# Performance work log

Measured on AMD Instinct MI355X. Metric: run time of the kernel, lower is better.

Reference implementation:

```python
import jax, jax.numpy as jnp
import numpy as np

B = 256        # trees per batch
DEPTH = 10     # complete binary tree depth -> 2^10 - 1 = 1023 internal nodes
N = 2**DEPTH - 1
IN = 128       # input_size
H = 128        # hidden_size
C = 5          # num_classes


def setup_inputs() -> dict:
    key = jax.random.key(0)
    ks = jax.random.split(key, 13)
    gdim = IN + 2 * H  # concat(x, h_left, h_right)
    inp = {"x": jax.random.normal(ks[0], (B, N, IN), jnp.float32)}
    names = ["i", "fl", "fr", "o", "u"]
    for j, nm in enumerate(names):
        inp[f"W_{nm}"] = 0.05 * jax.random.normal(ks[1 + 2 * j], (H, gdim), jnp.float32)
        inp[f"b_{nm}"] = 0.05 * jax.random.normal(ks[2 + 2 * j], (H,), jnp.float32)
    inp["W_cls"] = 0.05 * jax.random.normal(ks[11], (C, H), jnp.float32)
    inp["b_cls"] = 0.05 * jax.random.normal(ks[12], (C,), jnp.float32)
    return inp


def reference(x, W_i, b_i, W_fl, b_fl, W_fr, b_fr, W_o, b_o, W_u, b_u, W_cls, b_cls):
    # Level-order complete binary tree: node k has children 2k+1, 2k+2.
    # Bottom-up sweep; below the deepest internal level all children are
    # empty nodes with h = c = 0 (matches the original base case).
    Bb = x.shape[0]
    h = jnp.zeros((Bb, 2 ** DEPTH, H), x.dtype)
    c = jnp.zeros_like(h)
    for d in range(DEPTH - 1, -1, -1):  # fixed, small structural loop
        n = 2 ** d
        start = n - 1  # level-order offset of level d
        xs = x[:, start:start + n]            # [B, n, IN]
        hl, hr = h[:, 0::2], h[:, 1::2]       # children of node j are 2j, 2j+1 (level-local)
        cl, cr = c[:, 0::2], c[:, 1::2]
        comb = jnp.concatenate([xs, hl, hr], axis=-1)  # [B, n, IN+2H]
        lin = lambda W, b: jnp.einsum('bng,og->bno', comb, W) + b
        i = jax.nn.sigmoid(lin(W_i, b_i))
        fl = jax.nn.sigmoid(lin(W_fl, b_fl))
        fr = jax.nn.sigmoid(lin(W_fr, b_fr))
        o = jax.nn.sigmoid(lin(W_o, b_o))
        u = jnp.tanh(lin(W_u, b_u))
        c = i * u + fl * cl + fr * cr
        h = o * jnp.tanh(c)
    root_h = h[:, 0]                          # [B, H]
    logits = root_h @ W_cls.T + b_cls         # [B, C]
    return logits
```

## Files before the change

kernel.cpp:

```cpp
#include <hip/hip_runtime.h>
#include <hip/hip_bf16.h>
#include <stdint.h>


#define BATCH 256
#define NTOT 1023
#define HDIM 128
#define NCLS 5
#define GDIM 384

typedef __bf16 bf16x8 __attribute__((ext_vector_type(8)));
typedef float f32x4 __attribute__((ext_vector_type(4)));

__device__ __forceinline__ float sigmoid_f(float v) { return 1.f / (1.f + __expf(-v)); }
__device__ __forceinline__ float tanh_f(float v) { return 1.f - 2.f / (1.f + __expf(2.f * v)); }

__device__ __forceinline__ void load_lds16(const void* g, void* l) {
  __builtin_amdgcn_global_load_lds((const __attribute__((address_space(1))) unsigned int*)g,
                                   (__attribute__((address_space(3))) unsigned int*)l, 16, 0, 0);
}

__global__ __launch_bounds__(256) void pack_w(
    const float* __restrict__ W0, const float* __restrict__ W1, const float* __restrict__ W2,
    const float* __restrict__ W3, const float* __restrict__ W4, __bf16* __restrict__ PW)
{
  int t = blockIdx.x * 256 + threadIdx.x;
  int lane = t & 63;
  int chunk = t >> 6;
  int ks = chunk % 12;
  int jf = (chunk / 12) & 7;
  int g = chunk / 96;
  const float* W = (g == 0) ? W0 : (g == 1) ? W1 : (g == 2) ? W2 : (g == 3) ? W3 : W4;
  const float* s = W + (size_t)(jf * 16 + (lane & 15)) * GDIM + ks * 32 + (lane >> 4) * 8;
  float4 v0 = *(const float4*)s;
  float4 v1 = *(const float4*)(s + 4);
  bf16x8 w;
  w[0] = (__bf16)v0.x; w[1] = (__bf16)v0.y; w[2] = (__bf16)v0.z; w[3] = (__bf16)v0.w;
  w[4] = (__bf16)v1.x; w[5] = (__bf16)v1.y; w[6] = (__bf16)v1.z; w[7] = (__bf16)v1.w;
  *(bf16x8*)(PW + (size_t)t * 8) = w;
}

#define TB_P  81920
#define TB_Q  132096
#define CSTR  132

template<int NMF, bool LEAF, bool LAST>
__device__ __forceinline__ void fused_level(
    const float* __restrict__ xp,
    const __bf16* __restrict__ PW,
    const float* __restrict__ bv0, const float* __restrict__ bv1,
    const float* __restrict__ bv2, const float* __restrict__ bv3,
    const float* __restrict__ bv4,
    unsigned char* lds,
    const unsigned char* prev_h, const float* prev_c,
    unsigned char* cur_h, float* cur_c,
    __bf16* __restrict__ gh, float* __restrict__ gc,
    int nvalid)
{
  const int tid = threadIdx.x;
  const int w = tid >> 6;
  const int l = tid & 63;
  const int l15 = l & 15;
  const int quad = l >> 4;
  const int q8 = quad * 8;
  constexpr int NACC = LEAF ? 3 : 5;
  constexpr int NKT = LEAF ? 4 : 12;
  constexpr int NCH = NACC * 8;
  constexpr int NQ = NCH / 8;

  auto stageB = [&](int ks) {
    unsigned char* Bb = lds + (ks & 1) * 40960;
#pragma unroll
    for (int q = 0; q < NQ; ++q) {
      int c = w * NQ + q;
      int ai = c >> 3, jf = c & 7;
      int g = LEAF ? (ai ? ai + 2 : 0) : ai;
      const __bf16* src = PW + (((size_t)(g * 8 + jf) * 12 + ks) * 64 + l) * 8;
      load_lds16(src, Bb + c * 1024);
    }
  };

  stageB(0);

  bf16x8 xf[NMF][4];
#pragma unroll
  for (int mf = 0; mf < NMF; ++mf) {
    const float* xr = xp + (size_t)(mf * 16 + l15) * HDIM + q8;
#pragma unroll
    for (int kx = 0; kx < 4; ++kx) {
      float4 v0 = *(const float4*)(xr + kx * 32);
      float4 v1 = *(const float4*)(xr + kx * 32 + 4);
      bf16x8 t;
      t[0] = (__bf16)v0.x; t[1] = (__bf16)v0.y; t[2] = (__bf16)v0.z; t[3] = (__bf16)v0.w;
      t[4] = (__bf16)v1.x; t[5] = (__bf16)v1.y; t[6] = (__bf16)v1.z; t[7] = (__bf16)v1.w;
      xf[mf][kx] = t;
    }
  }

  f32x4 acc[NMF][NACC];
#pragma unroll
  for (int mf = 0; mf < NMF; ++mf)
#pragma unroll
    for (int ai = 0; ai < NACC; ++ai)
      acc[mf][ai] = (f32x4){0.f, 0.f, 0.f, 0.f};

#pragma unroll
  for (int ks = 0; ks < NKT; ++ks) {
    __syncthreads();
    if (ks + 1 < NKT) stageB(ks + 1);
    const unsigned char* Bb = lds + (ks & 1) * 40960;
    bf16x8 a[NMF];
#pragma unroll
    for (int mf = 0; mf < NMF; ++mf) {
      if (LEAF || ks < 4) {
        a[mf] = xf[mf][LEAF ? ks : (ks & 3)];
      } else {
        const int o = (ks < 8) ? 0 : 1;
        const int col2 = ((ks - (o ? 8 : 4)) * 32 + q8) * 2;
        const int n = 2 * (mf * 16 + l15) + o;
        a[mf] = *(const bf16x8*)(prev_h + n * 256 + (col2 ^ ((n & 7) << 4)));
      }
    }
#pragma unroll
    for (int ai = 0; ai < NACC; ++ai) {
      bf16x8 bb = *(const bf16x8*)(Bb + (ai * 8 + w) * 1024 + l * 16);
#pragma unroll
      for (int mf = 0; mf < NMF; ++mf)
        acc[mf][ai] = __builtin_amdgcn_mfma_f32_16x16x32_bf16(a[mf], bb, acc[mf][ai], 0, 0, 0);
    }
  }

  const int je = w * 16 + l15;
  const float b0 = bv0[je], b3v = bv3[je], b4v = bv4[je];
#pragma unroll
  for (int mf = 0; mf < NMF; ++mf) {
#pragma unroll
    for (int r = 0; r < 4; ++r) {
      const int me = mf * 16 + quad * 4 + r;
      if (me < nvalid) {
        float gi = sigmoid_f(acc[mf][0][r] + b0);
        float go = sigmoid_f(acc[mf][LEAF ? 1 : 3][r] + b3v);
        float gu = tanh_f(acc[mf][LEAF ? 2 : 4][r] + b4v);
        float cv = gi * gu;
        if constexpr (!LEAF) {
          float gl = sigmoid_f(acc[mf][1][r] + bv1[je]);
          float gr = sigmoid_f(acc[mf][2][r] + bv2[je]);
          cv += gl * prev_c[(2 * me) * CSTR + je] + gr * prev_c[(2 * me + 1) * CSTR + je];
        }
        float hv = go * tanh_f(cv);
        if constexpr (LAST) {
          gc[(size_t)me * HDIM + je] = cv;
          gh[(size_t)me * HDIM + je] = (__bf16)hv;
        } else {
          cur_c[me * CSTR + je] = cv;
          *(__bf16*)(cur_h + me * 256 + ((je * 2) ^ ((me & 7) << 4))) = (__bf16)hv;
        }
      }
    }
  }
}

__global__ __launch_bounds__(512, 1) void fused_top(
    const float* __restrict__ x, const __bf16* __restrict__ PW,
    const float* __restrict__ bv0, const float* __restrict__ bv1,
    const float* __restrict__ bv2, const float* __restrict__ bv3,
    const float* __restrict__ bv4,
    __bf16* __restrict__ h6, float* __restrict__ c6)
{
  __shared__ unsigned char lds[157184];
  const int b = blockIdx.x >> 3;
  const int s = blockIdx.x & 7;
  unsigned char* Ph = lds + TB_P;
  float* Pc = (float*)(lds + TB_P + 16384);
  unsigned char* Qh = lds + TB_Q;
  float* Qc = (float*)(lds + TB_Q + 8192);
  const size_t xb = (size_t)b * NTOT;

  fused_level<4, true, false>(x + (xb + 511 + s * 64) * HDIM, PW,
      bv0, bv1, bv2, bv3, bv4, lds, nullptr, nullptr, Ph, Pc, nullptr, nullptr, 64);
  fused_level<2, false, false>(x + (xb + 255 + s * 32) * HDIM, PW,
      bv0, bv1, bv2, bv3, bv4, lds, Ph, Pc, Qh, Qc, nullptr, nullptr, 32);
  fused_level<1, false, false>(x + (xb + 127 + s * 16) * HDIM, PW,
      bv0, bv1, bv2, bv3, bv4, lds, Qh, Qc, Ph, Pc, nullptr, nullptr, 16);
  fused_level<1, false, true>(x + (xb + 63 + s * 8) * HDIM, PW,
      bv0, bv1, bv2, bv3, bv4, lds, Ph, Pc, nullptr, nullptr,
      h6 + ((size_t)b * 64 + s * 8) * HDIM, c6 + ((size_t)b * 64 + s * 8) * HDIM, 8);
}

__global__ __launch_bounds__(256, 1) void tail_kernel(
    const float* __restrict__ x, const __bf16* __restrict__ PW,
    const float* __restrict__ bv0, const float* __restrict__ bv1,
    const float* __restrict__ bv2, const float* __restrict__ bv3,
    const float* __restrict__ bv4,
    const float* __restrict__ Wcls, const float* __restrict__ bcls,
    const __bf16* __restrict__ h6, const float* __restrict__ c6,
    float* __restrict__ out)
{
  __shared__ unsigned char lds[157184];
  const int b = blockIdx.x;
  const int tid = threadIdx.x;
  const int w = tid >> 6;
  const int l = tid & 63;
  const int l15 = l & 15;
  const int quad = l >> 4;
  const int q8 = quad * 8;

  unsigned char* Ph = lds + TB_P;
  float* Pc = (float*)(lds + TB_P + 16384);
  unsigned char* Qh = lds + TB_Q;
  float* Qc = (float*)(lds + TB_Q + 8192);

  {
    const __bf16* hs = h6 + (size_t)b * 64 * HDIM;
#pragma unroll
    for (int it = 0; it < 4; ++it) {
      int idx = it * 256 + tid;
      int node = idx >> 4, i8 = idx & 15;
      bf16x8 v = *(const bf16x8*)(hs + node * HDIM + i8 * 8);
      *(bf16x8*)(Ph + node * 256 + ((i8 * 16) ^ ((node & 7) << 4))) = v;
    }
    const float* cs = c6 + (size_t)b * 64 * HDIM;
#pragma unroll
    for (int it = 0; it < 8; ++it) {
      int idx = it * 256 + tid;
      int node = idx >> 5, seg = idx & 31;
      float4 v = *(const float4*)(cs + node * HDIM + seg * 4);
      *(float4*)(Pc + node * CSTR + seg * 4) = v;
    }
  }

  for (int d = 5; d >= 0; --d) {
    const int s = 5 - d;
    const int n = 1 << d;
    const int nmf = (d == 5) ? 2 : 1;
    unsigned char* prev_h = (s & 1) ? Qh : Ph;
    float*         prev_c = (s & 1) ? Qc : Pc;
    unsigned char* cur_h  = (s & 1) ? Ph : Qh;
    float*         cur_c  = (s & 1) ? Pc : Qc;

    bf16x8 xf[2][4];
#pragma unroll
    for (int mf = 0; mf < 2; ++mf) {
      const float* xr = x + ((size_t)b * NTOT + (n - 1) + mf * 16 + l15) * HDIM + q8;
#pragma unroll
      for (int ks = 0; ks < 4; ++ks) {
        float4 v0 = *(const float4*)(xr + ks * 32);
        float4 v1 = *(const float4*)(xr + ks * 32 + 4);
        bf16x8 t;
        t[0] = (__bf16)v0.x; t[1] = (__bf16)v0.y; t[2] = (__bf16)v0.z; t[3] = (__bf16)v0.w;
        t[4] = (__bf16)v1.x; t[5] = (__bf16)v1.y; t[6] = (__bf16)v1.z; t[7] = (__bf16)v1.w;
        xf[mf][ks] = t;
      }
    }

    auto stageB = [&](int ks) {
      unsigned char* Bb = lds + (ks & 1) * 40960;
#pragma unroll
      for (int q = 0; q < 10; ++q) {
        int c = w * 10 + q;
        const __bf16* src = PW + ((size_t)(c * 12 + ks) * 64 + l) * 8;
        load_lds16(src, Bb + c * 1024);
      }
    };

    f32x4 acc[2][2][5];
#pragma unroll
    for (int mf = 0; mf < 2; ++mf)
#pragma unroll
      for (int jfl = 0; jfl < 2; ++jfl)
#pragma unroll
        for (int g = 0; g < 5; ++g)
          acc[mf][jfl][g] = (f32x4){0.f, 0.f, 0.f, 0.f};

    stageB(0);
    for (int ks = 0; ks < 12; ++ks) {
      __syncthreads();
      if (ks < 11) stageB(ks + 1);
      const unsigned char* Bb = lds + (ks & 1) * 40960;
      bf16x8 a0, a1;
      if (ks < 4) {
        a0 = xf[0][ks];
        a1 = xf[1][ks];
      } else {
        const int o = (ks < 8) ? 0 : 1;
        const int col2 = (((ks - (o ? 8 : 4)) * 32) + q8) * 2;
        int n0 = 2 * l15 + o;
        int n1 = 2 * (16 + l15) + o;
        a0 = *(const bf16x8*)(prev_h + n0 * 256 + (col2 ^ ((n0 & 7) << 4)));
        a1 = *(const bf16x8*)(prev_h + n1 * 256 + (col2 ^ ((n1 & 7) << 4)));
      }
#pragma unroll
      for (int g = 0; g < 5; ++g) {
#pragma unroll
        for (int jfl = 0; jfl < 2; ++jfl) {
          bf16x8 bb = *(const bf16x8*)(Bb + (g * 8 + w * 2 + jfl) * 1024 + l * 16);
          acc[0][jfl][g] = __builtin_amdgcn_mfma_f32_16x16x32_bf16(a0, bb, acc[0][jfl][g], 0, 0, 0);
          if (nmf == 2)
            acc[1][jfl][g] = __builtin_amdgcn_mfma_f32_16x16x32_bf16(a1, bb, acc[1][jfl][g], 0, 0, 0);
        }
      }
    }

#pragma unroll
    for (int jfl = 0; jfl < 2; ++jfl) {
      const int je = w * 32 + jfl * 16 + l15;
      const float b0 = bv0[je], b1 = bv1[je], b2 = bv2[je], b3 = bv3[je], b4 = bv4[je];
#pragma unroll
      for (int mf = 0; mf < 2; ++mf) {
#pragma unroll
        for (int r = 0; r < 4; ++r) {
          const int me = mf * 16 + quad * 4 + r;
          if (me < n) {
            float gi = sigmoid_f(acc[mf][jfl][0][r] + b0);
            float gl = sigmoid_f(acc[mf][jfl][1][r] + b1);
            float gr = sigmoid_f(acc[mf][jfl][2][r] + b2);
            float go = sigmoid_f(acc[mf][jfl][3][r] + b3);
            float gu = tanh_f(acc[mf][jfl][4][r] + b4);
            float cv = gi * gu + gl * prev_c[(2 * me) * CSTR + je]
                               + gr * prev_c[(2 * me + 1) * CSTR + je];
            cur_c[me * CSTR + je] = cv;
            *(__bf16*)(cur_h + me * 256 + ((je * 2) ^ ((me & 7) << 4))) =
                (__bf16)(go * tanh_f(cv));
          }
        }
      }
    }
  }

  __syncthreads();
  if (tid < NCLS) {
    float sacc = bcls[tid];
    for (int k = 0; k < HDIM; ++k)
      sacc += (float)(*(const __bf16*)(Ph + k * 2)) * Wcls[tid * HDIM + k];
    out[(size_t)b * NCLS + tid] = sacc;
  }
}

extern "C" void kernel_launch(void* const* d_in, const int* in_sizes, int n_in,
                              void* d_out, int out_size, void* d_ws, size_t ws_size,
                              hipStream_t stream) {
  const float* x  = (const float*)d_in[0];
  const float* W[5]  = {(const float*)d_in[1], (const float*)d_in[3], (const float*)d_in[5],
                        (const float*)d_in[7], (const float*)d_in[9]};
  const float* bv[5] = {(const float*)d_in[2], (const float*)d_in[4], (const float*)d_in[6],
                        (const float*)d_in[8], (const float*)d_in[10]};
  const float* Wcls = (const float*)d_in[11];
  const float* bcls = (const float*)d_in[12];

  uint8_t* ws = (uint8_t*)d_ws;
  __bf16* hb1 = (__bf16*)(ws + 33554432);
  float*  cb1 = (float*)(ws + 117440512);
  __bf16* PW  = (__bf16*)(ws + 150994944);

  pack_w<<<120, 256, 0, stream>>>(W[0], W[1], W[2], W[3], W[4], PW);

  fused_top<<<BATCH * 8, 512, 0, stream>>>(
      x, PW, bv[0], bv[1], bv[2], bv[3], bv[4], hb1, cb1);

  tail_kernel<<<BATCH, 256, 0, stream>>>(
      x, PW, bv[0], bv[1], bv[2], bv[3], bv[4],
      Wcls, bcls, hb1, cb1, (float*)d_out);
}
```

Baseline: 565.7 us.

## Give each wave private double-buffered weight staging with vmcnt waits instead of block barriers

Each wave now stages into its own LDS region only the weight chunks it consumes, so the per-k-step __syncthreads is removed. Progress is tracked with explicit s_waitcnt vmcnt/lgkmcnt and the pipeline prefetches two k-steps ahead. Explicit barriers are added between levels so the h/c exchange stays correct. The intent is to remove block-wide synchronisation stalls in the MFMA loop and deepen load overlap, at the cost of relying on hand-counted wait numbers that must match the issued loads.

```diff
diff --git a/kernel.cpp b/kernel.cpp
--- a/kernel.cpp
+++ b/kernel.cpp
@@ -18,6 +18,16 @@
 __device__ __forceinline__ void load_lds16(const void* g, void* l) {
   __builtin_amdgcn_global_load_lds((const __attribute__((address_space(1))) unsigned int*)g,
                                    (__attribute__((address_space(3))) unsigned int*)l, 16, 0, 0);
+}
+
+template<int N>
+__device__ __forceinline__ void wait_vm() {
+  asm volatile("s_waitcnt vmcnt(%0)" :: "i"(N) : "memory");
+  __builtin_amdgcn_sched_barrier(0);
+}
+__device__ __forceinline__ void wait_lgkm0() {
+  asm volatile("s_waitcnt lgkmcnt(0)" ::: "memory");
+  __builtin_amdgcn_sched_barrier(0);
 }
 
 __global__ __launch_bounds__(256) void pack_w(
@@ -65,22 +75,20 @@
   const int q8 = quad * 8;
   constexpr int NACC = LEAF ? 3 : 5;
   constexpr int NKT = LEAF ? 4 : 12;
-  constexpr int NCH = NACC * 8;
-  constexpr int NQ = NCH / 8;
-
-  auto stageB = [&](int ks) {
-    unsigned char* Bb = lds + (ks & 1) * 40960;
-#pragma unroll
-    for (int q = 0; q < NQ; ++q) {
-      int c = w * NQ + q;
-      int ai = c >> 3, jf = c & 7;
-      int g = LEAF ? (ai ? ai + 2 : 0) : ai;
-      const __bf16* src = PW + (((size_t)(g * 8 + jf) * 12 + ks) * 64 + l) * 8;
-      load_lds16(src, Bb + c * 1024);
+  unsigned char* Bw = lds + w * 10240;
+
+  auto stage = [&](int ks) {
+    unsigned char* Bb = Bw + (ks & 1) * 5120;
+#pragma unroll
+    for (int q = 0; q < NACC; ++q) {
+      int g = LEAF ? (q ? q + 2 : 0) : q;
+      const __bf16* src = PW + (((size_t)(g * 8 + w) * 12 + ks) * 64 + l) * 8;
+      load_lds16(src, Bb + q * 1024);
     }
   };
 
-  stageB(0);
+  stage(0);
+  stage(1);
 
   bf16x8 xf[NMF][4];
 #pragma unroll
@@ -106,9 +114,12 @@
 
 #pragma unroll
   for (int ks = 0; ks < NKT; ++ks) {
-    __syncthreads();
-    if (ks + 1 < NKT) stageB(ks + 1);
-    const unsigned char* Bb = lds + (ks & 1) * 40960;
+    if (ks < NKT - 1) wait_vm<NACC>(); else wait_vm<0>();
+    const unsigned char* Bb = Bw + (ks & 1) * 5120;
+    bf16x8 bb[NACC];
+#pragma unroll
+    for (int q = 0; q < NACC; ++q)
+      bb[q] = *(const bf16x8*)(Bb + q * 1024 + l * 16);
     bf16x8 a[NMF];
 #pragma unroll
     for (int mf = 0; mf < NMF; ++mf) {
@@ -117,16 +128,18 @@
       } else {
         const int o = (ks < 8) ? 0 : 1;
         const int col2 = ((ks - (o ? 8 : 4)) * 32 + q8) * 2;
-        const int n = 2 * (mf * 16 + l15) + o;
-        a[mf] = *(const bf16x8*)(prev_h + n * 256 + (col2 ^ ((n & 7) << 4)));
-      }
-    }
-#pragma unroll
-    for (int ai = 0; ai < NACC; ++ai) {
-      bf16x8 bb = *(const bf16x8*)(Bb + (ai * 8 + w) * 1024 + l * 16);
+        const int nn = 2 * (mf * 16 + l15) + o;
+        a[mf] = *(const bf16x8*)(prev_h + nn * 256 + (col2 ^ ((nn & 7) << 4)));
+      }
+    }
+#pragma unroll
+    for (int q = 0; q < NACC; ++q)
 #pragma unroll
       for (int mf = 0; mf < NMF; ++mf)
-        acc[mf][ai] = __builtin_amdgcn_mfma_f32_16x16x32_bf16(a[mf], bb, acc[mf][ai], 0, 0, 0);
+        acc[mf][q] = __builtin_amdgcn_mfma_f32_16x16x32_bf16(a[mf], bb[q], acc[mf][q], 0, 0, 0);
+    if (ks + 2 < NKT) {
+      wait_lgkm0();
+      stage(ks + 2);
     }
   }
 
@@ -178,10 +191,13 @@
 
   fused_level<4, true, false>(x + (xb + 511 + s * 64) * HDIM, PW,
       bv0, bv1, bv2, bv3, bv4, lds, nullptr, nullptr, Ph, Pc, nullptr, nullptr, 64);
+  __syncthreads();
   fused_level<2, false, false>(x + (xb + 255 + s * 32) * HDIM, PW,
       bv0, bv1, bv2, bv3, bv4, lds, Ph, Pc, Qh, Qc, nullptr, nullptr, 32);
+  __syncthreads();
   fused_level<1, false, false>(x + (xb + 127 + s * 16) * HDIM, PW,
       bv0, bv1, bv2, bv3, bv4, lds, Qh, Qc, Ph, Pc, nullptr, nullptr, 16);
+  __syncthreads();
   fused_level<1, false, true>(x + (xb + 63 + s * 8) * HDIM, PW,
       bv0, bv1, bv2, bv3, bv4, lds, Ph, Pc, nullptr, nullptr,
       h6 + ((size_t)b * 64 + s * 8) * HDIM, c6 + ((size_t)b * 64 + s * 8) * HDIM, 8);
@@ -228,6 +244,7 @@
       *(float4*)(Pc + node * CSTR + seg * 4) = v;
     }
   }
+  __syncthreads();
 
   for (int d = 5; d >= 0; --d) {
     const int s = 5 - d;
@@ -237,6 +254,20 @@
     float*         prev_c = (s & 1) ? Qc : Pc;
     unsigned char* cur_h  = (s & 1) ? Ph : Qh;
     float*         cur_c  = (s & 1) ? Pc : Qc;
+    unsigned char* Bw = lds + w * 20480;
+
+    auto stageB = [&](int ks) {
+      unsigned char* Bb = Bw + (ks & 1) * 10240;
+#pragma unroll
+      for (int q = 0; q < 10; ++q) {
+        int g = q >> 1, jfl = q & 1;
+        const __bf16* src = PW + (((size_t)(g * 8 + w * 2 + jfl) * 12 + ks) * 64 + l) * 8;
+        load_lds16(src, Bb + q * 1024);
+      }
+    };
+
+    stageB(0);
+    stageB(1);
 
     bf16x8 xf[2][4];
 #pragma unroll
@@ -253,16 +284,6 @@
       }
     }
 
-    auto stageB = [&](int ks) {
-      unsigned char* Bb = lds + (ks & 1) * 40960;
-#pragma unroll
-      for (int q = 0; q < 10; ++q) {
-        int c = w * 10 + q;
-        const __bf16* src = PW + ((size_t)(c * 12 + ks) * 64 + l) * 8;
-        load_lds16(src, Bb + c * 1024);
-      }
-    };
-
     f32x4 acc[2][2][5];
 #pragma unroll
     for (int mf = 0; mf < 2; ++mf)
@@ -272,11 +293,10 @@
         for (int g = 0; g < 5; ++g)
           acc[mf][jfl][g] = (f32x4){0.f, 0.f, 0.f, 0.f};
 
-    stageB(0);
+#pragma unroll
     for (int ks = 0; ks < 12; ++ks) {
-      __syncthreads();
-      if (ks < 11) stageB(ks + 1);
-      const unsigned char* Bb = lds + (ks & 1) * 40960;
+      if (ks < 11) wait_vm<10>(); else wait_vm<0>();
+      const unsigned char* Bb = Bw + (ks & 1) * 10240;
       bf16x8 a0, a1;
       if (ks < 4) {
         a0 = xf[0][ks];
@@ -293,11 +313,15 @@
       for (int g = 0; g < 5; ++g) {
 #pragma unroll
         for (int jfl = 0; jfl < 2; ++jfl) {
-          bf16x8 bb = *(const bf16x8*)(Bb + (g * 8 + w * 2 + jfl) * 1024 + l * 16);
-          acc[0][jfl][g] = __builtin_amdgcn_mfma_f32_16x16x32_bf16(a0, bb, acc[0][jfl][g], 0, 0, 0);
+          bf16x8 bbv = *(const bf16x8*)(Bb + (g * 2 + jfl) * 1024 + l * 16);
+          acc[0][jfl][g] = __builtin_amdgcn_mfma_f32_16x16x32_bf16(a0, bbv, acc[0][jfl][g], 0, 0, 0);
           if (nmf == 2)
-            acc[1][jfl][g] = __builtin_amdgcn_mfma_f32_16x16x32_bf16(a1, bb, acc[1][jfl][g], 0, 0, 0);
+            acc[1][jfl][g] = __builtin_amdgcn_mfma_f32_16x16x32_bf16(a1, bbv, acc[1][jfl][g], 0, 0, 0);
         }
+      }
+      if (ks + 2 < 12) {
+        wait_lgkm0();
+        stageB(ks + 2);
       }
     }
 
@@ -325,9 +349,9 @@
         }
       }
     }
-  }
-
-  __syncthreads();
+    __syncthreads();
+  }
+
   if (tid < NCLS) {
     float sacc = bcls[tid];
     for (int k = 0; k < HDIM; ++k)
```

New measurement: 554.9 us. About the same (-1.9%).

## Load weight fragments directly into registers and shrink LDS to raise occupancy

Applied to the files above, without the earlier changes.

Weight B-fragments are no longer staged through double-buffered LDS via global_load_lds. Each wave now loads its fragments straight from global memory into registers, with a two-deep prefetch, and x fragments are streamed the same way. This cuts LDS use to about 75KB, so launch bounds can allow several blocks per CU, and the per-k-step __syncthreads is removed. The tail kernel is rewritten to 512 threads and reuses the shared fused_level routine. The risks are more register pressure and redundant weight loads from L2 across waves and blocks.

```diff
diff --git a/kernel.cpp b/kernel.cpp
--- a/kernel.cpp
+++ b/kernel.cpp
@@ -14,11 +14,6 @@
 
 __device__ __forceinline__ float sigmoid_f(float v) { return 1.f / (1.f + __expf(-v)); }
 __device__ __forceinline__ float tanh_f(float v) { return 1.f - 2.f / (1.f + __expf(2.f * v)); }
-
-__device__ __forceinline__ void load_lds16(const void* g, void* l) {
-  __builtin_amdgcn_global_load_lds((const __attribute__((address_space(1))) unsigned int*)g,
-                                   (__attribute__((address_space(3))) unsigned int*)l, 16, 0, 0);
-}
 
 __global__ __launch_bounds__(256) void pack_w(
     const float* __restrict__ W0, const float* __restrict__ W1, const float* __restrict__ W2,
@@ -40,9 +35,9 @@
   *(bf16x8*)(PW + (size_t)t * 8) = w;
 }
 
-#define TB_P  81920
-#define TB_Q  132096
-#define CSTR  132
+#define LDS_TOT 75264
+#define Q_OFF   50176
+#define CSTR    132
 
 template<int NMF, bool LEAF, bool LAST>
 __device__ __forceinline__ void fused_level(
@@ -51,7 +46,6 @@
     const float* __restrict__ bv0, const float* __restrict__ bv1,
     const float* __restrict__ bv2, const float* __restrict__ bv3,
     const float* __restrict__ bv4,
-    unsigned char* lds,
     const unsigned char* prev_h, const float* prev_c,
     unsigned char* cur_h, float* cur_c,
     __bf16* __restrict__ gh, float* __restrict__ gc,
@@ -65,69 +59,66 @@
   const int q8 = quad * 8;
   constexpr int NACC = LEAF ? 3 : 5;
   constexpr int NKT = LEAF ? 4 : 12;
-  constexpr int NCH = NACC * 8;
-  constexpr int NQ = NCH / 8;
-
-  auto stageB = [&](int ks) {
-    unsigned char* Bb = lds + (ks & 1) * 40960;
-#pragma unroll
-    for (int q = 0; q < NQ; ++q) {
-      int c = w * NQ + q;
-      int ai = c >> 3, jf = c & 7;
-      int g = LEAF ? (ai ? ai + 2 : 0) : ai;
-      const __bf16* src = PW + (((size_t)(g * 8 + jf) * 12 + ks) * 64 + l) * 8;
-      load_lds16(src, Bb + c * 1024);
+
+  const bf16x8* PB = (const bf16x8*)PW;
+
+  bf16x8 bb[2][NACC];
+  bf16x8 xb[2][NMF];
+
+  auto loadB = [&](int buf, int ks) {
+#pragma unroll
+    for (int q = 0; q < NACC; ++q) {
+      const int g = LEAF ? (q ? q + 2 : 0) : q;
+      bb[buf][q] = PB[((size_t)(g * 8 + w) * 12 + ks) * 64 + l];
     }
   };
-
-  stageB(0);
-
-  bf16x8 xf[NMF][4];
-#pragma unroll
-  for (int mf = 0; mf < NMF; ++mf) {
-    const float* xr = xp + (size_t)(mf * 16 + l15) * HDIM + q8;
-#pragma unroll
-    for (int kx = 0; kx < 4; ++kx) {
-      float4 v0 = *(const float4*)(xr + kx * 32);
-      float4 v1 = *(const float4*)(xr + kx * 32 + 4);
+  auto loadX = [&](int buf, int kx) {
+#pragma unroll
+    for (int mf = 0; mf < NMF; ++mf) {
+      const float* xr = xp + (size_t)(mf * 16 + l15) * HDIM + q8 + kx * 32;
+      float4 v0 = *(const float4*)xr;
+      float4 v1 = *(const float4*)(xr + 4);
       bf16x8 t;
       t[0] = (__bf16)v0.x; t[1] = (__bf16)v0.y; t[2] = (__bf16)v0.z; t[3] = (__bf16)v0.w;
       t[4] = (__bf16)v1.x; t[5] = (__bf16)v1.y; t[6] = (__bf16)v1.z; t[7] = (__bf16)v1.w;
-      xf[mf][kx] = t;
-    }
-  }
+      xb[buf][mf] = t;
+    }
+  };
+
+  loadB(0, 0);
+  loadX(0, 0);
+  loadB(1, 1);
+  loadX(1, 1);
 
   f32x4 acc[NMF][NACC];
 #pragma unroll
   for (int mf = 0; mf < NMF; ++mf)
 #pragma unroll
-    for (int ai = 0; ai < NACC; ++ai)
-      acc[mf][ai] = (f32x4){0.f, 0.f, 0.f, 0.f};
+    for (int q = 0; q < NACC; ++q)
+      acc[mf][q] = (f32x4){0.f, 0.f, 0.f, 0.f};
 
 #pragma unroll
   for (int ks = 0; ks < NKT; ++ks) {
-    __syncthreads();
-    if (ks + 1 < NKT) stageB(ks + 1);
-    const unsigned char* Bb = lds + (ks & 1) * 40960;
+    const int cb = ks & 1;
     bf16x8 a[NMF];
 #pragma unroll
     for (int mf = 0; mf < NMF; ++mf) {
       if (LEAF || ks < 4) {
-        a[mf] = xf[mf][LEAF ? ks : (ks & 3)];
+        a[mf] = xb[cb][mf];
       } else {
         const int o = (ks < 8) ? 0 : 1;
         const int col2 = ((ks - (o ? 8 : 4)) * 32 + q8) * 2;
-        const int n = 2 * (mf * 16 + l15) + o;
-        a[mf] = *(const bf16x8*)(prev_h + n * 256 + (col2 ^ ((n & 7) << 4)));
+        const int nn = 2 * (mf * 16 + l15) + o;
+        a[mf] = *(const bf16x8*)(prev_h + nn * 256 + (col2 ^ ((nn & 7) << 4)));
       }
     }
 #pragma unroll
-    for (int ai = 0; ai < NACC; ++ai) {
-      bf16x8 bb = *(const bf16x8*)(Bb + (ai * 8 + w) * 1024 + l * 16);
+    for (int q = 0; q < NACC; ++q)
 #pragma unroll
       for (int mf = 0; mf < NMF; ++mf)
-        acc[mf][ai] = __builtin_amdgcn_mfma_f32_16x16x32_bf16(a[mf], bb, acc[mf][ai], 0, 0, 0);
-    }
+        acc[mf][q] = __builtin_amdgcn_mfma_f32_16x16x32_bf16(a[mf], bb[cb][q], acc[mf][q], 0, 0, 0);
+    if (ks + 2 < NKT) loadB(cb, ks + 2);
+    if (ks + 2 < 4)   loadX(cb, ks + 2);
   }
 
   const int je = w * 16 + l15;
@@ -160,34 +151,37 @@
   }
 }
 
-__global__ __launch_bounds__(512, 1) void fused_top(
+__global__ __launch_bounds__(512, 4) void fused_top(
     const float* __restrict__ x, const __bf16* __restrict__ PW,
     const float* __restrict__ bv0, const float* __restrict__ bv1,
     const float* __restrict__ bv2, const float* __restrict__ bv3,
     const float* __restrict__ bv4,
     __bf16* __restrict__ h6, float* __restrict__ c6)
 {
-  __shared__ unsigned char lds[157184];
+  __shared__ unsigned char lds[LDS_TOT];
   const int b = blockIdx.x >> 3;
   const int s = blockIdx.x & 7;
-  unsigned char* Ph = lds + TB_P;
-  float* Pc = (float*)(lds + TB_P + 16384);
-  unsigned char* Qh = lds + TB_Q;
-  float* Qc = (float*)(lds + TB_Q + 8192);
+  unsigned char* Ph = lds;
+  float* Pc = (float*)(lds + 16384);
+  unsigned char* Qh = lds + Q_OFF;
+  float* Qc = (float*)(lds + Q_OFF + 8192);
   const size_t xb = (size_t)b * NTOT;
 
   fused_level<4, true, false>(x + (xb + 511 + s * 64) * HDIM, PW,
-      bv0, bv1, bv2, bv3, bv4, lds, nullptr, nullptr, Ph, Pc, nullptr, nullptr, 64);
+      bv0, bv1, bv2, bv3, bv4, nullptr, nullptr, Ph, Pc, nullptr, nullptr, 64);
+  __syncthreads();
   fused_level<2, false, false>(x + (xb + 255 + s * 32) * HDIM, PW,
-      bv0, bv1, bv2, bv3, bv4, lds, Ph, Pc, Qh, Qc, nullptr, nullptr, 32);
+      bv0, bv1, bv2, bv3, bv4, Ph, Pc, Qh, Qc, nullptr, nullptr, 32);
+  __syncthreads();
   fused_level<1, false, false>(x + (xb + 127 + s * 16) * HDIM, PW,
-      bv0, bv1, bv2, bv3, bv4, lds, Qh, Qc, Ph, Pc, nullptr, nullptr, 16);
+      bv0, bv1, bv2, bv3, bv4, Qh, Qc, Ph, Pc, nullptr, nullptr, 16);
+  __syncthreads();
   fused_level<1, false, true>(x + (xb + 63 + s * 8) * HDIM, PW,
-      bv0, bv1, bv2, bv3, bv4, lds, Ph, Pc, nullptr, nullptr,
+      bv0, bv1, bv2, bv3, bv4, Ph, Pc, nullptr, nullptr,
       h6 + ((size_t)b * 64 + s * 8) * HDIM, c6 + ((size_t)b * 64 + s * 8) * HDIM, 8);
 }
 
-__global__ __launch_bounds__(256, 1) void tail_kernel(
+__global__ __launch_bounds__(512, 4) void tail_kernel(
     const float* __restrict__ x, const __bf16* __restrict__ PW,
     const float* __restrict__ bv0, const float* __restrict__ bv1,
     const float* __restrict__ bv2, const float* __restrict__ bv3,
@@ -196,138 +190,54 @@
     const __bf16* __restrict__ h6, const float* __restrict__ c6,
     float* __restrict__ out)
 {
-  __shared__ unsigned char lds[157184];
+  __shared__ unsigned char lds[LDS_TOT];
   const int b = blockIdx.x;
   const int tid = threadIdx.x;
-  const int w = tid >> 6;
-  const int l = tid & 63;
-  const int l15 = l & 15;
-  const int quad = l >> 4;
-  const int q8 = quad * 8;
-
-  unsigned char* Ph = lds + TB_P;
-  float* Pc = (float*)(lds + TB_P + 16384);
-  unsigned char* Qh = lds + TB_Q;
-  float* Qc = (float*)(lds + TB_Q + 8192);
+  unsigned char* Ph = lds;
+  float* Pc = (float*)(lds + 16384);
+  unsigned char* Qh = lds + Q_OFF;
+  float* Qc = (float*)(lds + Q_OFF + 8192);
 
   {
     const __bf16* hs = h6 + (size_t)b * 64 * HDIM;
 #pragma unroll
-    for (int it = 0; it < 4; ++it) {
-      int idx = it * 256 + tid;
+    for (int it = 0; it < 2; ++it) {
+      int idx = it * 512 + tid;
       int node = idx >> 4, i8 = idx & 15;
       bf16x8 v = *(const bf16x8*)(hs + node * HDIM + i8 * 8);
       *(bf16x8*)(Ph + node * 256 + ((i8 * 16) ^ ((node & 7) << 4))) = v;
     }
     const float* cs = c6 + (size_t)b * 64 * HDIM;
 #pragma unroll
-    for (int it = 0; it < 8; ++it) {
-      int idx = it * 256 + tid;
+    for (int it = 0; it < 4; ++it) {
+      int idx = it * 512 + tid;
       int node = idx >> 5, seg = idx & 31;
       float4 v = *(const float4*)(cs + node * HDIM + seg * 4);
       *(float4*)(Pc + node * CSTR + seg * 4) = v;
     }
   }
-
-  for (int d = 5; d >= 0; --d) {
-    const int s = 5 - d;
-    const int n = 1 << d;
-    const int nmf = (d == 5) ? 2 : 1;
-    unsigned char* prev_h = (s & 1) ? Qh : Ph;
-    float*         prev_c = (s & 1) ? Qc : Pc;
-    unsigned char* cur_h  = (s & 1) ? Ph : Qh;
-    float*         cur_c  = (s & 1) ? Pc : Qc;
-
-    bf16x8 xf[2][4];
-#pragma unroll
-    for (int mf = 0; mf < 2; ++mf) {
-      const float* xr = x + ((size_t)b * NTOT + (n - 1) + mf * 16 + l15) * HDIM + q8;
-#pragma unroll
-      for (int ks = 0; ks < 4; ++ks) {
-        float4 v0 = *(const float4*)(xr + ks * 32);
-        float4 v1 = *(const float4*)(xr + ks * 32 + 4);
-        bf16x8 t;
-        t[0] = (__bf16)v0.x; t[1] = (__bf16)v0.y; t[2] = (__bf16)v0.z; t[3] = (__bf16)v0.w;
-        t[4] = (__bf16)v1.x; t[5] = (__bf16)v1.y; t[6] = (__bf16)v1.z; t[7] = (__bf16)v1.w;
-        xf[mf][ks] = t;
-      }
-    }
-
-    auto stageB = [&](int ks) {
-      unsigned char* Bb = lds + (ks & 1) * 40960;
-#pragma unroll
-      for (int q = 0; q < 10; ++q) {
-        int c = w * 10 + q;
-        const __bf16* src = PW + ((size_t)(c * 12 + ks) * 64 + l) * 8;
-        load_lds16(src, Bb + c * 1024);
-      }
-    };
-
-    f32x4 acc[2][2][5];
-#pragma unroll
-    for (int mf = 0; mf < 2; ++mf)
-#pragma unroll
-      for (int jfl = 0; jfl < 2; ++jfl)
-#pragma unroll
-        for (int g = 0; g < 5; ++g)
-          acc[mf][jfl][g] = (f32x4){0.f, 0.f, 0.f, 0.f};
-
-    stageB(0);
-    for (int ks = 0; ks < 12; ++ks) {
-      __syncthreads();
-      if (ks < 11) stageB(ks + 1);
-      const unsigned char* Bb = lds + (ks & 1) * 40960;
-      bf16x8 a0, a1;
-      if (ks < 4) {
-        a0 = xf[0][ks];
-        a1 = xf[1][ks];
-      } else {
-        const int o = (ks < 8) ? 0 : 1;
-        const int col2 = (((ks - (o ? 8 : 4)) * 32) + q8) * 2;
-        int n0 = 2 * l15 + o;
-        int n1 = 2 * (16 + l15) + o;
-        a0 = *(const bf16x8*)(prev_h + n0 * 256 + (col2 ^ ((n0 & 7) << 4)));
-        a1 = *(const bf16x8*)(prev_h + n1 * 256 + (col2 ^ ((n1 & 7) << 4)));
-      }
-#pragma unroll
-      for (int g = 0; g < 5; ++g) {
-#pragma unroll
-        for (int jfl = 0; jfl < 2; ++jfl) {
-          bf16x8 bb = *(const bf16x8*)(Bb + (g * 8 + w * 2 + jfl) * 1024 + l * 16);
-          acc[0][jfl][g] = __builtin_amdgcn_mfma_f32_16x16x32_bf16(a0, bb, acc[0][jfl][g], 0, 0, 0);
-          if (nmf == 2)
-            acc[1][jfl][g] = __builtin_amdgcn_mfma_f32_16x16x32_bf16(a1, bb, acc[1][jfl][g], 0, 0, 0);
-        }
-      }
-    }
-
-#pragma unroll
-    for (int jfl = 0; jfl < 2; ++jfl) {
-      const int je = w * 32 + jfl * 16 + l15;
-      const float b0 = bv0[je], b1 = bv1[je], b2 = bv2[je], b3 = bv3[je], b4 = bv4[je];
-#pragma unroll
-      for (int mf = 0; mf < 2; ++mf) {
-#pragma unroll
-        for (int r = 0; r < 4; ++r) {
-          const int me = mf * 16 + quad * 4 + r;
-          if (me < n) {
-            float gi = sigmoid_f(acc[mf][jfl][0][r] + b0);
-            float gl = sigmoid_f(acc[mf][jfl][1][r] + b1);
-            float gr = sigmoid_f(acc[mf][jfl][2][r] + b2);
-            float go = sigmoid_f(acc[mf][jfl][3][r] + b3);
-            float gu = tanh_f(acc[mf][jfl][4][r] + b4);
-            float cv = gi * gu + gl * prev_c[(2 * me) * CSTR + je]
-                               + gr * prev_c[(2 * me + 1) * CSTR + je];
-            cur_c[me * CSTR + je] = cv;
-            *(__bf16*)(cur_h + me * 256 + ((je * 2) ^ ((me & 7) << 4))) =
-                (__bf16)(go * tanh_f(cv));
-          }
-        }
-      }
-    }
-  }
-
-  __syncthreads();
+  __syncthreads();
+
+  const size_t xb = (size_t)b * NTOT;
+  fused_level<2, false, false>(x + (xb + 31) * HDIM, PW,
+      bv0, bv1, bv2, bv3, bv4, Ph, Pc, Qh, Qc, nullptr, nullptr, 32);
+  __syncthreads();
+  fused_level<1, false, false>(x + (xb + 15) * HDIM, PW,
+      bv0, bv1, bv2, bv3, bv4, Qh, Qc, Ph, Pc, nullptr, nullptr, 16);
+  __syncthreads();
+  fused_level<1, false, false>(x + (xb + 7) * HDIM, PW,
+      bv0, bv1, bv2, bv3, bv4, Ph, Pc, Qh, Qc, nullptr, nullptr, 8);
+  __syncthreads();
+  fused_level<1, false, false>(x + (xb + 3) * HDIM, PW,
+      bv0, bv1, bv2, bv3, bv4, Qh, Qc, Ph, Pc, nullptr, nullptr, 4);
+  __syncthreads();
+  fused_level<1, false, false>(x + (xb + 1) * HDIM, PW,
+      bv0, bv1, bv2, bv3, bv4, Ph, Pc, Qh, Qc, nullptr, nullptr, 2);
+  __syncthreads();
+  fused_level<1, false, false>(x + (xb + 0) * HDIM, PW,
+      bv0, bv1, bv2, bv3, bv4, Qh, Qc, Ph, Pc, nullptr, nullptr, 1);
+  __syncthreads();
+
   if (tid < NCLS) {
     float sacc = bcls[tid];
     for (int k = 0; k < HDIM; ++k)
@@ -357,7 +267,7 @@
   fused_top<<<BATCH * 8, 512, 0, stream>>>(
       x, PW, bv[0], bv[1], bv[2], bv[3], bv[4], hb1, cb1);
 
-  tail_kernel<<<BATCH, 256, 0, stream>>>(
+  tail_kernel<<<BATCH, 512, 0, stream>>>(
       x, PW, bv[0], bv[1], bv[2], bv[3], bv[4],
       Wcls, bcls, hb1, cb1, (float*)d_out);
 }
```

New measurement: 544.6 us. 3.7% less time.
